# Kernel optimization log

Measured on AMD Instinct MI355X. Metric: run time of the kernel, lower is better.

Reference implementation:

```python
import jax, jax.numpy as jnp
import numpy as np

NUM_EMBEDDINGS = 1024
EMBEDDING_DIM = 64


def setup_inputs() -> dict:
    key = jax.random.key(0)
    k1, k2 = jax.random.split(key)
    z = jax.random.normal(k1, (64, 32, 32, EMBEDDING_DIM), dtype=jnp.float32)
    # torch init: uniform_(-1/num_embeddings, 1/num_embeddings)
    lim = 1.0 / NUM_EMBEDDINGS
    codebook = jax.random.uniform(
        k2, (NUM_EMBEDDINGS, EMBEDDING_DIM), dtype=jnp.float32,
        minval=-lim, maxval=lim)
    return {"z": z, "codebook": codebook}


def reference(z, codebook):
    # z: [..., D]; codebook: [K, D]
    z_flat = z.reshape(-1, z.shape[-1])                      # [N, D]
    # ||z||^2 - 2 z.e + ||e||^2  -> [N, K]
    distances = (
        jnp.sum(z_flat ** 2, axis=1, keepdims=True)
        - 2.0 * jnp.einsum("nd,kd->nk", z_flat, codebook)
        + jnp.sum(codebook ** 2, axis=1)
    )
    min_indices = jnp.argmin(distances, axis=1)              # [N]
    z_q = jnp.take(codebook, min_indices, axis=0).reshape(z.shape)
    return z_q, min_indices
```

## Files before the change

### kernel.cpp

```cpp
#include <hip/hip_runtime.h>
#include <hip/hip_bf16.h>
#include <math.h>


#define D      64
#define K      1024
#define BLOCK  256

typedef _Float16 half8_t __attribute__((ext_vector_type(8)));
typedef float    floatx4 __attribute__((ext_vector_type(4)));

#define WS_CN_OFF    0
#define WS_EF_OFF    4096

__device__ __forceinline__ void gld_lds16(const void* g, void* l) {
    __builtin_amdgcn_global_load_lds(
        (const __attribute__((address_space(1))) void*)g,
        (__attribute__((address_space(3))) void*)l, 16, 0, 0);
}

__device__ __forceinline__ float np_sumsq64_p(const float* __restrict__ x) {
    float r[8];
    {
        float4 v0 = *(const float4*)(x);
        float4 v1 = *(const float4*)(x + 4);
        r[0] = __fmul_rn(v0.x, v0.x); r[1] = __fmul_rn(v0.y, v0.y);
        r[2] = __fmul_rn(v0.z, v0.z); r[3] = __fmul_rn(v0.w, v0.w);
        r[4] = __fmul_rn(v1.x, v1.x); r[5] = __fmul_rn(v1.y, v1.y);
        r[6] = __fmul_rn(v1.z, v1.z); r[7] = __fmul_rn(v1.w, v1.w);
    }
#pragma unroll
    for (int i = 8; i < 64; i += 8) {
        float4 v0 = *(const float4*)(x + i);
        float4 v1 = *(const float4*)(x + i + 4);
        r[0] = __fadd_rn(r[0], __fmul_rn(v0.x, v0.x));
        r[1] = __fadd_rn(r[1], __fmul_rn(v0.y, v0.y));
        r[2] = __fadd_rn(r[2], __fmul_rn(v0.z, v0.z));
        r[3] = __fadd_rn(r[3], __fmul_rn(v0.w, v0.w));
        r[4] = __fadd_rn(r[4], __fmul_rn(v1.x, v1.x));
        r[5] = __fadd_rn(r[5], __fmul_rn(v1.y, v1.y));
        r[6] = __fadd_rn(r[6], __fmul_rn(v1.z, v1.z));
        r[7] = __fadd_rn(r[7], __fmul_rn(v1.w, v1.w));
    }
    return __fadd_rn(__fadd_rn(__fadd_rn(r[0], r[1]), __fadd_rn(r[2], r[3])),
                     __fadd_rn(__fadd_rn(r[4], r[5]), __fadd_rn(r[6], r[7])));
}

__global__ void vq_pre(const float* __restrict__ cb, float* __restrict__ cn,
                       _Float16* __restrict__ ef) {
    const int k = blockIdx.x * 64 + threadIdx.x;
    if (k >= K) return;
    cn[k] = np_sumsq64_p(cb + (long)k * D);
    const int t = k >> 6, ct = (k >> 4) & 3, l16 = k & 15;
#pragma unroll
    for (int ch = 0; ch < 2; ++ch)
#pragma unroll
        for (int quad = 0; quad < 4; ++quad) {
            const float* p = cb + (long)k * D + ch * 32 + quad * 8;
            half8_t h1, h2;
#pragma unroll
            for (int j = 0; j < 8; ++j) {
                float x10 = __fmul_rn(p[j], 1024.0f);
                _Float16 g1 = (_Float16)x10;
                h1[j] = g1;
                h2[j] = (_Float16)(__fmul_rn(__fsub_rn(x10, (float)g1), 2048.0f));
            }
            const int base = t * 8192 + 128 * quad + 8 * l16;
            *(half8_t*)(ef + base + 512 * (ch * 4 + ct))       = h1;
            *(half8_t*)(ef + base + 512 * ((2 + ch) * 4 + ct)) = h2;
        }
}

__global__ __launch_bounds__(BLOCK, 2) void vq_main(
    const float* __restrict__ z, const float* __restrict__ cb,
    const _Float16* __restrict__ ef, const float* __restrict__ cn,
    float* __restrict__ zq, float* __restrict__ idx_out) {
    __shared__ __align__(16) char smem[34816];
    __shared__ float sS[128];
    __shared__ float sCn[K];
    __shared__ int   sBi[128];
    float*    zf   = (float*)smem;
    _Float16* bufs = (_Float16*)smem;

    const int tid  = threadIdx.x;
    const int lane = tid & 63;
    const int wv   = tid >> 6;
    const int quad = lane >> 4;
    const int l16  = lane & 15;
    const long rowbase = (long)blockIdx.x * 128;

    const float4* gz = (const float4*)(z + rowbase * D);
#pragma unroll
    for (int i = 0; i < 8; ++i) {
        int idx4 = i * BLOCK + tid;
        int r = idx4 >> 4, j = idx4 & 15;
        *(float4*)(zf + r * 68 + j * 4) = gz[idx4];
    }
#pragma unroll
    for (int i = 0; i < 4; ++i) sCn[i * 256 + tid] = cn[i * 256 + tid];
    __syncthreads();

    if (tid < 128) sS[tid] = np_sumsq64_p(zf + tid * 68);

    half8_t a1[2][2], a2[2][2];
#pragma unroll
    for (int rt = 0; rt < 2; ++rt) {
        const int row = wv * 32 + rt * 16 + l16;
#pragma unroll
        for (int ch = 0; ch < 2; ++ch) {
            const float* p = zf + row * 68 + ch * 32 + quad * 8;
            float4 f0 = *(const float4*)(p);
            float4 f1 = *(const float4*)(p + 4);
            float xs[8] = {f0.x, f0.y, f0.z, f0.w, f1.x, f1.y, f1.z, f1.w};
#pragma unroll
            for (int j = 0; j < 8; ++j) {
                _Float16 h1 = (_Float16)xs[j];
                a1[rt][ch][j] = h1;
                a2[rt][ch][j] =
                    (_Float16)(__fmul_rn(__fsub_rn(xs[j], (float)h1), 2048.0f));
            }
        }
    }
    __syncthreads();

    float myS[2][4];
#pragma unroll
    for (int rt = 0; rt < 2; ++rt)
#pragma unroll
        for (int r = 0; r < 4; ++r)
            myS[rt][r] = sS[wv * 32 + rt * 16 + quad * 4 + r];

    float bv[2][4];
    int   bi[2][4];
#pragma unroll
    for (int rt = 0; rt < 2; ++rt)
#pragma unroll
        for (int r = 0; r < 4; ++r) { bv[rt][r] = INFINITY; bi[rt][r] = 0; }

    const char* eb = (const char*)ef;

    {
        const char* g = eb + wv * 4096 + lane * 16;
        char* l = (char*)bufs + wv * 4096;
#pragma unroll
        for (int i = 0; i < 4; ++i) gld_lds16(g + i * 1024, l + i * 1024);
    }
    __syncthreads();

    for (int t = 0; t < 16; ++t) {
        const _Float16* cur = bufs + (t & 1) * 8192;
        if (t < 15) {
            const char* g = eb + (t + 1) * 16384 + wv * 4096 + lane * 16;
            char* l = (char*)bufs + ((t + 1) & 1) * 16384 + wv * 4096;
#pragma unroll
            for (int i = 0; i < 4; ++i) gld_lds16(g + i * 1024, l + i * 1024);
        }

        const _Float16* tb = cur + 8 * lane;
        const int kbase = t * 64;
#pragma unroll
        for (int ct = 0; ct < 4; ++ct) {
            half8_t b1[2], b2[2];
#pragma unroll
            for (int ch = 0; ch < 2; ++ch) {
                b1[ch] = *(const half8_t*)(tb + 512 * (ch * 4 + ct));
                b2[ch] = *(const half8_t*)(tb + 512 * ((2 + ch) * 4 + ct));
            }
            const float cnv = sCn[kbase + ct * 16 + l16];
            const int kg = kbase + ct * 16 + l16;
#pragma unroll
            for (int rt = 0; rt < 2; ++rt) {
                floatx4 aM = (floatx4){0.f, 0.f, 0.f, 0.f};
                floatx4 aC = (floatx4){0.f, 0.f, 0.f, 0.f};
                aM = __builtin_amdgcn_mfma_f32_16x16x32_f16(a1[rt][0], b1[0], aM, 0, 0, 0);
                aM = __builtin_amdgcn_mfma_f32_16x16x32_f16(a1[rt][1], b1[1], aM, 0, 0, 0);
                aC = __builtin_amdgcn_mfma_f32_16x16x32_f16(a1[rt][0], b2[0], aC, 0, 0, 0);
                aC = __builtin_amdgcn_mfma_f32_16x16x32_f16(a1[rt][1], b2[1], aC, 0, 0, 0);
                aC = __builtin_amdgcn_mfma_f32_16x16x32_f16(a2[rt][0], b1[0], aC, 0, 0, 0);
                aC = __builtin_amdgcn_mfma_f32_16x16x32_f16(a2[rt][1], b1[1], aC, 0, 0, 0);
#pragma unroll
                for (int r = 0; r < 4; ++r) {
                    float ds = fmaf(aC[r], 0x1p-11f, aM[r]);
                    float t2 = __fmul_rn(ds, 0x1p-9f);
                    float dist = __fadd_rn(__fsub_rn(myS[rt][r], t2), cnv);
                    if (dist < bv[rt][r]) { bv[rt][r] = dist; bi[rt][r] = kg; }
                }
            }
        }
        __syncthreads();
    }

#pragma unroll
    for (int rt = 0; rt < 2; ++rt)
#pragma unroll
        for (int r = 0; r < 4; ++r) {
            float v = bv[rt][r];
            int   x = bi[rt][r];
#pragma unroll
            for (int off = 1; off <= 8; off <<= 1) {
                float ov = __shfl_xor(v, off);
                int   ox = __shfl_xor(x, off);
                if (ov < v || (ov == v && ox < x)) { v = ov; x = ox; }
            }
            if (l16 == 0) {
                const int rl = wv * 32 + rt * 16 + quad * 4 + r;
                sBi[rl] = x;
                idx_out[rowbase + rl] = (float)x;
            }
        }
    __syncthreads();

    const float4* cb4 = (const float4*)cb;
    float4* zq4 = (float4*)(zq + rowbase * D);
#pragma unroll
    for (int i = 0; i < 8; ++i) {
        int idx4 = i * BLOCK + tid;
        int r = idx4 >> 4, j = idx4 & 15;
        zq4[idx4] = cb4[(long)sBi[r] * 16 + j];
    }
}

extern "C" void kernel_launch(void* const* d_in, const int* in_sizes, int n_in,
                              void* d_out, int out_size, void* d_ws, size_t ws_size,
                              hipStream_t stream) {
    const float* z  = (const float*)d_in[0];
    const float* cb = (const float*)d_in[1];

    const int n_rows = in_sizes[0] / D;
    float* zq      = (float*)d_out;
    float* idx_out = zq + (long)n_rows * D;

    float*    ws_cn = (float*)((char*)d_ws + WS_CN_OFF);
    _Float16* ws_ef = (_Float16*)((char*)d_ws + WS_EF_OFF);

    vq_pre<<<K / 64, 64, 0, stream>>>(cb, ws_cn, ws_ef);
    vq_main<<<n_rows / 128, BLOCK, 0, stream>>>(z, cb, ws_ef, ws_cn, zq, idx_out);
}
```

Baseline: 101.7 us.

## Software-pipeline MFMA groups with delayed epilogue across codebook tiles

Restructures the inner codebook loop so that two sets of accumulators alternate: the MFMAs for one 16-column chunk are issued while the distance/argmin epilogue of the previous chunk runs. The last chunk's epilogue is carried across the tile barrier into the next iteration. LDS B loads are also issued ahead of their MFMAs. The aim is to hide MFMA latency and LDS read latency behind VALU work. The cost is more live VGPRs and a dummy first epilogue that is seeded with -inf accumulators, which yields +inf distances so nothing is selected.

```diff
diff --git a/kernel.cpp b/kernel.cpp
--- a/kernel.cpp
+++ b/kernel.cpp
@@ -145,10 +145,62 @@
 #pragma unroll
         for (int i = 0; i < 4; ++i) gld_lds16(g + i * 1024, l + i * 1024);
     }
-    __syncthreads();
-
+
+    half8_t b1A[2], b2A[2], b1B[2], b2B[2];
+    floatx4 aMA0, aMA1, aCA0, aCA1, aMB0, aMB1, aCB0, aCB1;
+    float cnv0, cnv1, cnv2, cnv3;
+
+    {
+        const floatx4 NI = {-INFINITY, -INFINITY, -INFINITY, -INFINITY};
+        const floatx4 Z4 = {0.f, 0.f, 0.f, 0.f};
+        aMB0 = NI; aMB1 = NI; aCB0 = Z4; aCB1 = Z4;
+        cnv3 = 0.f;
+    }
+
+#define LOADB(b1_, b2_, cnv_, t_, ct_) do {                                   \
+        const _Float16* tb_ = bufs + ((t_) & 1) * 8192 + 8 * lane;            \
+        b1_[0] = *(const half8_t*)(tb_ + 512 * (0 * 4 + (ct_)));              \
+        b1_[1] = *(const half8_t*)(tb_ + 512 * (1 * 4 + (ct_)));              \
+        b2_[0] = *(const half8_t*)(tb_ + 512 * (2 * 4 + (ct_)));              \
+        b2_[1] = *(const half8_t*)(tb_ + 512 * (3 * 4 + (ct_)));              \
+        cnv_ = sCn[(t_) * 64 + (ct_) * 16 + l16];                             \
+    } while (0)
+
+#define MFMAG(aM0_, aM1_, aC0_, aC1_, b1_, b2_) do {                          \
+        const floatx4 Z4_ = {0.f, 0.f, 0.f, 0.f};                             \
+        aM0_ = __builtin_amdgcn_mfma_f32_16x16x32_f16(a1[0][0], b1_[0], Z4_, 0, 0, 0); \
+        aM1_ = __builtin_amdgcn_mfma_f32_16x16x32_f16(a1[1][0], b1_[0], Z4_, 0, 0, 0); \
+        aM0_ = __builtin_amdgcn_mfma_f32_16x16x32_f16(a1[0][1], b1_[1], aM0_, 0, 0, 0); \
+        aM1_ = __builtin_amdgcn_mfma_f32_16x16x32_f16(a1[1][1], b1_[1], aM1_, 0, 0, 0); \
+        aC0_ = __builtin_amdgcn_mfma_f32_16x16x32_f16(a1[0][0], b2_[0], Z4_, 0, 0, 0); \
+        aC1_ = __builtin_amdgcn_mfma_f32_16x16x32_f16(a1[1][0], b2_[0], Z4_, 0, 0, 0); \
+        aC0_ = __builtin_amdgcn_mfma_f32_16x16x32_f16(a1[0][1], b2_[1], aC0_, 0, 0, 0); \
+        aC1_ = __builtin_amdgcn_mfma_f32_16x16x32_f16(a1[1][1], b2_[1], aC1_, 0, 0, 0); \
+        aC0_ = __builtin_amdgcn_mfma_f32_16x16x32_f16(a2[0][0], b1_[0], aC0_, 0, 0, 0); \
+        aC1_ = __builtin_amdgcn_mfma_f32_16x16x32_f16(a2[1][0], b1_[0], aC1_, 0, 0, 0); \
+        aC0_ = __builtin_amdgcn_mfma_f32_16x16x32_f16(a2[0][1], b1_[1], aC0_, 0, 0, 0); \
+        aC1_ = __builtin_amdgcn_mfma_f32_16x16x32_f16(a2[1][1], b1_[1], aC1_, 0, 0, 0); \
+    } while (0)
+
+#define EPI(aM0_, aM1_, aC0_, aC1_, cnv_, kb_) do {                           \
+        const int kg_ = (kb_) + l16;                                          \
+        _Pragma("unroll")                                                     \
+        for (int r = 0; r < 4; ++r) {                                         \
+            float ds0_ = fmaf(aC0_[r], 0x1p-11f, aM0_[r]);                    \
+            float d0_ = __fadd_rn(__fsub_rn(myS[0][r],                        \
+                            __fmul_rn(ds0_, 0x1p-9f)), cnv_);                 \
+            if (d0_ < bv[0][r]) { bv[0][r] = d0_; bi[0][r] = kg_; }           \
+            float ds1_ = fmaf(aC1_[r], 0x1p-11f, aM1_[r]);                    \
+            float d1_ = __fadd_rn(__fsub_rn(myS[1][r],                        \
+                            __fmul_rn(ds1_, 0x1p-9f)), cnv_);                 \
+            if (d1_ < bv[1][r]) { bv[1][r] = d1_; bi[1][r] = kg_; }           \
+        }                                                                     \
+    } while (0)
+
+    __syncthreads();
+
+#pragma unroll 2
     for (int t = 0; t < 16; ++t) {
-        const _Float16* cur = bufs + (t & 1) * 8192;
         if (t < 15) {
             const char* g = eb + (t + 1) * 16384 + wv * 4096 + lane * 16;
             char* l = (char*)bufs + ((t + 1) & 1) * 16384 + wv * 4096;
@@ -156,39 +208,25 @@
             for (int i = 0; i < 4; ++i) gld_lds16(g + i * 1024, l + i * 1024);
         }
 
-        const _Float16* tb = cur + 8 * lane;
-        const int kbase = t * 64;
-#pragma unroll
-        for (int ct = 0; ct < 4; ++ct) {
-            half8_t b1[2], b2[2];
-#pragma unroll
-            for (int ch = 0; ch < 2; ++ch) {
-                b1[ch] = *(const half8_t*)(tb + 512 * (ch * 4 + ct));
-                b2[ch] = *(const half8_t*)(tb + 512 * ((2 + ch) * 4 + ct));
-            }
-            const float cnv = sCn[kbase + ct * 16 + l16];
-            const int kg = kbase + ct * 16 + l16;
-#pragma unroll
-            for (int rt = 0; rt < 2; ++rt) {
-                floatx4 aM = (floatx4){0.f, 0.f, 0.f, 0.f};
-                floatx4 aC = (floatx4){0.f, 0.f, 0.f, 0.f};
-                aM = __builtin_amdgcn_mfma_f32_16x16x32_f16(a1[rt][0], b1[0], aM, 0, 0, 0);
-                aM = __builtin_amdgcn_mfma_f32_16x16x32_f16(a1[rt][1], b1[1], aM, 0, 0, 0);
-                aC = __builtin_amdgcn_mfma_f32_16x16x32_f16(a1[rt][0], b2[0], aC, 0, 0, 0);
-                aC = __builtin_amdgcn_mfma_f32_16x16x32_f16(a1[rt][1], b2[1], aC, 0, 0, 0);
-                aC = __builtin_amdgcn_mfma_f32_16x16x32_f16(a2[rt][0], b1[0], aC, 0, 0, 0);
-                aC = __builtin_amdgcn_mfma_f32_16x16x32_f16(a2[rt][1], b1[1], aC, 0, 0, 0);
-#pragma unroll
-                for (int r = 0; r < 4; ++r) {
-                    float ds = fmaf(aC[r], 0x1p-11f, aM[r]);
-                    float t2 = __fmul_rn(ds, 0x1p-9f);
-                    float dist = __fadd_rn(__fsub_rn(myS[rt][r], t2), cnv);
-                    if (dist < bv[rt][r]) { bv[rt][r] = dist; bi[rt][r] = kg; }
-                }
-            }
-        }
+        LOADB(b1A, b2A, cnv0, t, 0);
+        LOADB(b1B, b2B, cnv1, t, 1);
+        EPI(aMB0, aMB1, aCB0, aCB1, cnv3, (t - 1) * 64 + 48);
+        MFMAG(aMA0, aMA1, aCA0, aCA1, b1A, b2A);
+        LOADB(b1A, b2A, cnv2, t, 2);
+        MFMAG(aMB0, aMB1, aCB0, aCB1, b1B, b2B);
+        LOADB(b1B, b2B, cnv3, t, 3);
+        EPI(aMA0, aMA1, aCA0, aCA1, cnv0, t * 64 + 0);
+        MFMAG(aMA0, aMA1, aCA0, aCA1, b1A, b2A);
+        EPI(aMB0, aMB1, aCB0, aCB1, cnv1, t * 64 + 16);
+        MFMAG(aMB0, aMB1, aCB0, aCB1, b1B, b2B);
+        EPI(aMA0, aMA1, aCA0, aCA1, cnv2, t * 64 + 32);
         __syncthreads();
     }
+    EPI(aMB0, aMB1, aCB0, aCB1, cnv3, 15 * 64 + 48);
+
+#undef LOADB
+#undef MFMAG
+#undef EPI
 
 #pragma unroll
     for (int rt = 0; rt < 2; ++rt)
```

Result: no change. 102.2 us (+0.5%).

## Split codebook column tiles across waves with cross-wave argmin reduction

Applied to the files above, without the earlier changes.

Blocks now handle 64 rows with 512 threads. Each of 8 waves owns one 16-column codebook slice (ct) for one 32-row group, instead of each wave looping over all 4 column tiles. Per-wave partial argmins are merged through shared memory in a new reduction step. This doubles the block count and waves per row, aiming for better latency hiding and occupancy, at the cost of more codebook LDS traffic per row and an extra reduction pass with a barrier.

```diff
diff --git a/kernel.cpp b/kernel.cpp
--- a/kernel.cpp
+++ b/kernel.cpp
@@ -5,7 +5,8 @@
 
 #define D      64
 #define K      1024
-#define BLOCK  256
+#define BLOCK  512
+#define ROWS   64
 
 typedef _Float16 half8_t __attribute__((ext_vector_type(8)));
 typedef float    floatx4 __attribute__((ext_vector_type(4)));
@@ -71,41 +72,45 @@
         }
 }
 
-__global__ __launch_bounds__(BLOCK, 2) void vq_main(
+__global__ __launch_bounds__(BLOCK, 4) void vq_main(
     const float* __restrict__ z, const float* __restrict__ cb,
     const _Float16* __restrict__ ef, const float* __restrict__ cn,
     float* __restrict__ zq, float* __restrict__ idx_out) {
-    __shared__ __align__(16) char smem[34816];
-    __shared__ float sS[128];
+    __shared__ __align__(16) char smem[32768];
+    __shared__ float sS[ROWS];
     __shared__ float sCn[K];
-    __shared__ int   sBi[128];
+    __shared__ int   sBi[ROWS];
+    __shared__ float sRv[4][ROWS];
+    __shared__ int   sRi[4][ROWS];
     float*    zf   = (float*)smem;
     _Float16* bufs = (_Float16*)smem;
 
     const int tid  = threadIdx.x;
     const int lane = tid & 63;
     const int wv   = tid >> 6;
+    const int ct   = wv & 3;
+    const int rg   = wv >> 2;
     const int quad = lane >> 4;
     const int l16  = lane & 15;
-    const long rowbase = (long)blockIdx.x * 128;
+    const long rowbase = (long)blockIdx.x * ROWS;
 
     const float4* gz = (const float4*)(z + rowbase * D);
 #pragma unroll
-    for (int i = 0; i < 8; ++i) {
+    for (int i = 0; i < 2; ++i) {
         int idx4 = i * BLOCK + tid;
         int r = idx4 >> 4, j = idx4 & 15;
         *(float4*)(zf + r * 68 + j * 4) = gz[idx4];
     }
 #pragma unroll
-    for (int i = 0; i < 4; ++i) sCn[i * 256 + tid] = cn[i * 256 + tid];
-    __syncthreads();
-
-    if (tid < 128) sS[tid] = np_sumsq64_p(zf + tid * 68);
+    for (int i = 0; i < 2; ++i) sCn[i * BLOCK + tid] = cn[i * BLOCK + tid];
+    __syncthreads();
+
+    if (tid < ROWS) sS[tid] = np_sumsq64_p(zf + tid * 68);
 
     half8_t a1[2][2], a2[2][2];
 #pragma unroll
     for (int rt = 0; rt < 2; ++rt) {
-        const int row = wv * 32 + rt * 16 + l16;
+        const int row = rg * 32 + rt * 16 + l16;
 #pragma unroll
         for (int ch = 0; ch < 2; ++ch) {
             const float* p = zf + row * 68 + ch * 32 + quad * 8;
@@ -128,7 +133,7 @@
     for (int rt = 0; rt < 2; ++rt)
 #pragma unroll
         for (int r = 0; r < 4; ++r)
-            myS[rt][r] = sS[wv * 32 + rt * 16 + quad * 4 + r];
+            myS[rt][r] = sS[rg * 32 + rt * 16 + quad * 4 + r];
 
     float bv[2][4];
     int   bi[2][4];
@@ -140,52 +145,56 @@
     const char* eb = (const char*)ef;
 
     {
-        const char* g = eb + wv * 4096 + lane * 16;
-        char* l = (char*)bufs + wv * 4096;
-#pragma unroll
-        for (int i = 0; i < 4; ++i) gld_lds16(g + i * 1024, l + i * 1024);
-    }
-    __syncthreads();
-
+        const char* g = eb + wv * 2048 + lane * 16;
+        char* l = (char*)bufs + wv * 2048;
+#pragma unroll
+        for (int i = 0; i < 2; ++i) gld_lds16(g + i * 1024, l + i * 1024);
+    }
+    __syncthreads();
+
+#pragma unroll 2
     for (int t = 0; t < 16; ++t) {
-        const _Float16* cur = bufs + (t & 1) * 8192;
         if (t < 15) {
-            const char* g = eb + (t + 1) * 16384 + wv * 4096 + lane * 16;
-            char* l = (char*)bufs + ((t + 1) & 1) * 16384 + wv * 4096;
-#pragma unroll
-            for (int i = 0; i < 4; ++i) gld_lds16(g + i * 1024, l + i * 1024);
-        }
-
-        const _Float16* tb = cur + 8 * lane;
-        const int kbase = t * 64;
-#pragma unroll
-        for (int ct = 0; ct < 4; ++ct) {
-            half8_t b1[2], b2[2];
-#pragma unroll
-            for (int ch = 0; ch < 2; ++ch) {
-                b1[ch] = *(const half8_t*)(tb + 512 * (ch * 4 + ct));
-                b2[ch] = *(const half8_t*)(tb + 512 * ((2 + ch) * 4 + ct));
-            }
-            const float cnv = sCn[kbase + ct * 16 + l16];
-            const int kg = kbase + ct * 16 + l16;
-#pragma unroll
-            for (int rt = 0; rt < 2; ++rt) {
-                floatx4 aM = (floatx4){0.f, 0.f, 0.f, 0.f};
-                floatx4 aC = (floatx4){0.f, 0.f, 0.f, 0.f};
-                aM = __builtin_amdgcn_mfma_f32_16x16x32_f16(a1[rt][0], b1[0], aM, 0, 0, 0);
-                aM = __builtin_amdgcn_mfma_f32_16x16x32_f16(a1[rt][1], b1[1], aM, 0, 0, 0);
-                aC = __builtin_amdgcn_mfma_f32_16x16x32_f16(a1[rt][0], b2[0], aC, 0, 0, 0);
-                aC = __builtin_amdgcn_mfma_f32_16x16x32_f16(a1[rt][1], b2[1], aC, 0, 0, 0);
-                aC = __builtin_amdgcn_mfma_f32_16x16x32_f16(a2[rt][0], b1[0], aC, 0, 0, 0);
-                aC = __builtin_amdgcn_mfma_f32_16x16x32_f16(a2[rt][1], b1[1], aC, 0, 0, 0);
-#pragma unroll
-                for (int r = 0; r < 4; ++r) {
-                    float ds = fmaf(aC[r], 0x1p-11f, aM[r]);
-                    float t2 = __fmul_rn(ds, 0x1p-9f);
-                    float dist = __fadd_rn(__fsub_rn(myS[rt][r], t2), cnv);
-                    if (dist < bv[rt][r]) { bv[rt][r] = dist; bi[rt][r] = kg; }
-                }
-            }
+            const char* g = eb + (t + 1) * 16384 + wv * 2048 + lane * 16;
+            char* l = (char*)bufs + ((t + 1) & 1) * 16384 + wv * 2048;
+#pragma unroll
+            for (int i = 0; i < 2; ++i) gld_lds16(g + i * 1024, l + i * 1024);
+        }
+
+        const _Float16* tb = bufs + (t & 1) * 8192 + 8 * lane;
+        half8_t b1[2], b2[2];
+        b1[0] = *(const half8_t*)(tb + 512 * (0 * 4 + ct));
+        b1[1] = *(const half8_t*)(tb + 512 * (1 * 4 + ct));
+        b2[0] = *(const half8_t*)(tb + 512 * (2 * 4 + ct));
+        b2[1] = *(const half8_t*)(tb + 512 * (3 * 4 + ct));
+        const int kg  = t * 64 + ct * 16 + l16;
+        const float cnv = sCn[kg];
+
+        const floatx4 Z4 = {0.f, 0.f, 0.f, 0.f};
+        floatx4 aM0, aM1, aC0, aC1;
+        aM0 = __builtin_amdgcn_mfma_f32_16x16x32_f16(a1[0][0], b1[0], Z4, 0, 0, 0);
+        aM1 = __builtin_amdgcn_mfma_f32_16x16x32_f16(a1[1][0], b1[0], Z4, 0, 0, 0);
+        aM0 = __builtin_amdgcn_mfma_f32_16x16x32_f16(a1[0][1], b1[1], aM0, 0, 0, 0);
+        aM1 = __builtin_amdgcn_mfma_f32_16x16x32_f16(a1[1][1], b1[1], aM1, 0, 0, 0);
+        aC0 = __builtin_amdgcn_mfma_f32_16x16x32_f16(a1[0][0], b2[0], Z4, 0, 0, 0);
+        aC1 = __builtin_amdgcn_mfma_f32_16x16x32_f16(a1[1][0], b2[0], Z4, 0, 0, 0);
+        aC0 = __builtin_amdgcn_mfma_f32_16x16x32_f16(a1[0][1], b2[1], aC0, 0, 0, 0);
+        aC1 = __builtin_amdgcn_mfma_f32_16x16x32_f16(a1[1][1], b2[1], aC1, 0, 0, 0);
+        aC0 = __builtin_amdgcn_mfma_f32_16x16x32_f16(a2[0][0], b1[0], aC0, 0, 0, 0);
+        aC1 = __builtin_amdgcn_mfma_f32_16x16x32_f16(a2[1][0], b1[0], aC1, 0, 0, 0);
+        aC0 = __builtin_amdgcn_mfma_f32_16x16x32_f16(a2[0][1], b1[1], aC0, 0, 0, 0);
+        aC1 = __builtin_amdgcn_mfma_f32_16x16x32_f16(a2[1][1], b1[1], aC1, 0, 0, 0);
+
+#pragma unroll
+        for (int r = 0; r < 4; ++r) {
+            float ds0 = fmaf(aC0[r], 0x1p-11f, aM0[r]);
+            float t20 = __fmul_rn(ds0, 0x1p-9f);
+            float d0  = __fadd_rn(__fsub_rn(myS[0][r], t20), cnv);
+            if (d0 < bv[0][r]) { bv[0][r] = d0; bi[0][r] = kg; }
+            float ds1 = fmaf(aC1[r], 0x1p-11f, aM1[r]);
+            float t21 = __fmul_rn(ds1, 0x1p-9f);
+            float d1  = __fadd_rn(__fsub_rn(myS[1][r], t21), cnv);
+            if (d1 < bv[1][r]) { bv[1][r] = d1; bi[1][r] = kg; }
         }
         __syncthreads();
     }
@@ -203,17 +212,31 @@
                 if (ov < v || (ov == v && ox < x)) { v = ov; x = ox; }
             }
             if (l16 == 0) {
-                const int rl = wv * 32 + rt * 16 + quad * 4 + r;
-                sBi[rl] = x;
-                idx_out[rowbase + rl] = (float)x;
-            }
-        }
+                const int row = rg * 32 + rt * 16 + quad * 4 + r;
+                sRv[ct][row] = v;
+                sRi[ct][row] = x;
+            }
+        }
+    __syncthreads();
+
+    if (tid < ROWS) {
+        float v = sRv[0][tid];
+        int   x = sRi[0][tid];
+#pragma unroll
+        for (int c = 1; c < 4; ++c) {
+            float ov = sRv[c][tid];
+            int   ox = sRi[c][tid];
+            if (ov < v || (ov == v && ox < x)) { v = ov; x = ox; }
+        }
+        sBi[tid] = x;
+        idx_out[rowbase + tid] = (float)x;
+    }
     __syncthreads();
 
     const float4* cb4 = (const float4*)cb;
     float4* zq4 = (float4*)(zq + rowbase * D);
 #pragma unroll
-    for (int i = 0; i < 8; ++i) {
+    for (int i = 0; i < 2; ++i) {
         int idx4 = i * BLOCK + tid;
         int r = idx4 >> 4, j = idx4 & 15;
         zq4[idx4] = cb4[(long)sBi[r] * 16 + j];
@@ -234,5 +257,5 @@
     _Float16* ws_ef = (_Float16*)((char*)d_ws + WS_EF_OFF);
 
     vq_pre<<<K / 64, 64, 0, stream>>>(cb, ws_cn, ws_ef);
-    vq_main<<<n_rows / 128, BLOCK, 0, stream>>>(z, cb, ws_ef, ws_cn, zq, idx_out);
-}
+    vq_main<<<n_rows / ROWS, BLOCK, 0, stream>>>(z, cb, ws_ef, ws_cn, zq, idx_out);
+}
```

New measurement: 107.9 us. 1.06x slower.

## Load codebook fragments directly from global into registers, drop LDS staging

Applied to the files above, without the earlier changes.

Reorders the precomputed fp16 codebook layout so each 16-code group is a contiguous 4KB chunk, then has every wave load its B fragments straight from global/L2 into registers with a two-deep software prefetch. This removes the global_load_lds staging, the LDS reads, and the per-tile block barriers, and interleaves the two row-tile MFMA chains for more independence. The trade-off is that all four waves fetch the same codebook data redundantly through cache, and load latency is hidden only by register double buffering. LDS use also drops, which may allow more resident blocks.

```diff
diff --git a/kernel.cpp b/kernel.cpp
--- a/kernel.cpp
+++ b/kernel.cpp
@@ -12,12 +12,6 @@
 
 #define WS_CN_OFF    0
 #define WS_EF_OFF    4096
-
-__device__ __forceinline__ void gld_lds16(const void* g, void* l) {
-    __builtin_amdgcn_global_load_lds(
-        (const __attribute__((address_space(1))) void*)g,
-        (__attribute__((address_space(3))) void*)l, 16, 0, 0);
-}
 
 __device__ __forceinline__ float np_sumsq64_p(const float* __restrict__ x) {
     float r[8];
@@ -65,9 +59,9 @@
                 h1[j] = g1;
                 h2[j] = (_Float16)(__fmul_rn(__fsub_rn(x10, (float)g1), 2048.0f));
             }
-            const int base = t * 8192 + 128 * quad + 8 * l16;
-            *(half8_t*)(ef + base + 512 * (ch * 4 + ct))       = h1;
-            *(half8_t*)(ef + base + 512 * ((2 + ch) * 4 + ct)) = h2;
+            const int base = t * 8192 + ct * 2048 + 128 * quad + 8 * l16;
+            *(half8_t*)(ef + base + 512 * (ch))       = h1;
+            *(half8_t*)(ef + base + 512 * (2 + ch))   = h2;
         }
 }
 
@@ -75,12 +69,10 @@
     const float* __restrict__ z, const float* __restrict__ cb,
     const _Float16* __restrict__ ef, const float* __restrict__ cn,
     float* __restrict__ zq, float* __restrict__ idx_out) {
-    __shared__ __align__(16) char smem[34816];
+    __shared__ __align__(16) float zf[128 * 68];
     __shared__ float sS[128];
     __shared__ float sCn[K];
     __shared__ int   sBi[128];
-    float*    zf   = (float*)smem;
-    _Float16* bufs = (_Float16*)smem;
 
     const int tid  = threadIdx.x;
     const int lane = tid & 63;
@@ -137,58 +129,57 @@
 #pragma unroll
         for (int r = 0; r < 4; ++r) { bv[rt][r] = INFINITY; bi[rt][r] = 0; }
 
-    const char* eb = (const char*)ef;
-
-    {
-        const char* g = eb + wv * 4096 + lane * 16;
-        char* l = (char*)bufs + wv * 4096;
-#pragma unroll
-        for (int i = 0; i < 4; ++i) gld_lds16(g + i * 1024, l + i * 1024);
-    }
-    __syncthreads();
-
-    for (int t = 0; t < 16; ++t) {
-        const _Float16* cur = bufs + (t & 1) * 8192;
-        if (t < 15) {
-            const char* g = eb + (t + 1) * 16384 + wv * 4096 + lane * 16;
-            char* l = (char*)bufs + ((t + 1) & 1) * 16384 + wv * 4096;
-#pragma unroll
-            for (int i = 0; i < 4; ++i) gld_lds16(g + i * 1024, l + i * 1024);
-        }
-
-        const _Float16* tb = cur + 8 * lane;
-        const int kbase = t * 64;
-#pragma unroll
-        for (int ct = 0; ct < 4; ++ct) {
-            half8_t b1[2], b2[2];
-#pragma unroll
-            for (int ch = 0; ch < 2; ++ch) {
-                b1[ch] = *(const half8_t*)(tb + 512 * (ch * 4 + ct));
-                b2[ch] = *(const half8_t*)(tb + 512 * ((2 + ch) * 4 + ct));
-            }
-            const float cnv = sCn[kbase + ct * 16 + l16];
-            const int kg = kbase + ct * 16 + l16;
-#pragma unroll
-            for (int rt = 0; rt < 2; ++rt) {
-                floatx4 aM = (floatx4){0.f, 0.f, 0.f, 0.f};
-                floatx4 aC = (floatx4){0.f, 0.f, 0.f, 0.f};
-                aM = __builtin_amdgcn_mfma_f32_16x16x32_f16(a1[rt][0], b1[0], aM, 0, 0, 0);
-                aM = __builtin_amdgcn_mfma_f32_16x16x32_f16(a1[rt][1], b1[1], aM, 0, 0, 0);
-                aC = __builtin_amdgcn_mfma_f32_16x16x32_f16(a1[rt][0], b2[0], aC, 0, 0, 0);
-                aC = __builtin_amdgcn_mfma_f32_16x16x32_f16(a1[rt][1], b2[1], aC, 0, 0, 0);
-                aC = __builtin_amdgcn_mfma_f32_16x16x32_f16(a2[rt][0], b1[0], aC, 0, 0, 0);
-                aC = __builtin_amdgcn_mfma_f32_16x16x32_f16(a2[rt][1], b1[1], aC, 0, 0, 0);
-#pragma unroll
-                for (int r = 0; r < 4; ++r) {
-                    float ds = fmaf(aC[r], 0x1p-11f, aM[r]);
-                    float t2 = __fmul_rn(ds, 0x1p-9f);
-                    float dist = __fadd_rn(__fsub_rn(myS[rt][r], t2), cnv);
-                    if (dist < bv[rt][r]) { bv[rt][r] = dist; bi[rt][r] = kg; }
-                }
-            }
-        }
-        __syncthreads();
-    }
+    const char* eb = (const char*)ef + 16 * lane;
+
+#define LOADG(b1_, b2_, g_) do {                                              \
+        const char* p_ = eb + (size_t)(g_) * 4096;                            \
+        b1_[0] = *(const half8_t*)(p_);                                       \
+        b1_[1] = *(const half8_t*)(p_ + 1024);                                \
+        b2_[0] = *(const half8_t*)(p_ + 2048);                                \
+        b2_[1] = *(const half8_t*)(p_ + 3072);                                \
+    } while (0)
+
+#define COMPUTE(b1_, b2_, g_) do {                                            \
+        const int   kg_  = (g_) * 16 + l16;                                   \
+        const float cnv_ = sCn[kg_];                                          \
+        const floatx4 Z4_ = {0.f, 0.f, 0.f, 0.f};                             \
+        floatx4 aM0, aM1, aC0, aC1;                                           \
+        aM0 = __builtin_amdgcn_mfma_f32_16x16x32_f16(a1[0][0], b1_[0], Z4_, 0, 0, 0); \
+        aM1 = __builtin_amdgcn_mfma_f32_16x16x32_f16(a1[1][0], b1_[0], Z4_, 0, 0, 0); \
+        aM0 = __builtin_amdgcn_mfma_f32_16x16x32_f16(a1[0][1], b1_[1], aM0, 0, 0, 0); \
+        aM1 = __builtin_amdgcn_mfma_f32_16x16x32_f16(a1[1][1], b1_[1], aM1, 0, 0, 0); \
+        aC0 = __builtin_amdgcn_mfma_f32_16x16x32_f16(a1[0][0], b2_[0], Z4_, 0, 0, 0); \
+        aC1 = __builtin_amdgcn_mfma_f32_16x16x32_f16(a1[1][0], b2_[0], Z4_, 0, 0, 0); \
+        aC0 = __builtin_amdgcn_mfma_f32_16x16x32_f16(a1[0][1], b2_[1], aC0, 0, 0, 0); \
+        aC1 = __builtin_amdgcn_mfma_f32_16x16x32_f16(a1[1][1], b2_[1], aC1, 0, 0, 0); \
+        aC0 = __builtin_amdgcn_mfma_f32_16x16x32_f16(a2[0][0], b1_[0], aC0, 0, 0, 0); \
+        aC1 = __builtin_amdgcn_mfma_f32_16x16x32_f16(a2[1][0], b1_[0], aC1, 0, 0, 0); \
+        aC0 = __builtin_amdgcn_mfma_f32_16x16x32_f16(a2[0][1], b1_[1], aC0, 0, 0, 0); \
+        aC1 = __builtin_amdgcn_mfma_f32_16x16x32_f16(a2[1][1], b1_[1], aC1, 0, 0, 0); \
+        _Pragma("unroll")                                                     \
+        for (int r = 0; r < 4; ++r) {                                         \
+            float ds0 = fmaf(aC0[r], 0x1p-11f, aM0[r]);                       \
+            float d0  = __fadd_rn(__fsub_rn(myS[0][r],                        \
+                            __fmul_rn(ds0, 0x1p-9f)), cnv_);                  \
+            if (d0 < bv[0][r]) { bv[0][r] = d0; bi[0][r] = kg_; }             \
+            float ds1 = fmaf(aC1[r], 0x1p-11f, aM1[r]);                       \
+            float d1  = __fadd_rn(__fsub_rn(myS[1][r],                        \
+                            __fmul_rn(ds1, 0x1p-9f)), cnv_);                  \
+            if (d1 < bv[1][r]) { bv[1][r] = d1; bi[1][r] = kg_; }             \
+        }                                                                     \
+    } while (0)
+
+    half8_t b1A[2], b2A[2], b1B[2], b2B[2];
+    LOADG(b1A, b2A, 0);
+    for (int g = 0; g < 64; g += 2) {
+        LOADG(b1B, b2B, g + 1);
+        COMPUTE(b1A, b2A, g);
+        if (g < 62) LOADG(b1A, b2A, g + 2);
+        COMPUTE(b1B, b2B, g + 1);
+    }
+
+#undef LOADG
+#undef COMPUTE
 
 #pragma unroll
     for (int rt = 0; rt < 2; ++rt)
```

Result: no change. 102.0 us (+0.2%).
